# Kernel optimization log

Hardware: AMD Instinct MI355X
Metric: run time of the kernel (lower is better)

## Reference

```python
import jax, jax.numpy as jnp
import numpy as np

B, D = 256, 128            # batch, irreps_in dim for i='32x0e+32x1o' (32 + 32*3)
Z = D * (D + 1) // 2       # irreps_out.dim for symmetric formula 'ij=ji' -> 8256


def setup_inputs() -> dict:
    key = jax.random.key(0)
    k1, k2, k3 = jax.random.split(key, 3)
    x = jax.random.normal(k1, (B, D), dtype=jnp.float32)
    y = jax.random.normal(k2, (B, D), dtype=jnp.float32)
    # Precomputed change-of-basis (stand-in for the Wigner-3j/CG-built buffer).
    # Symmetrized over (i, j) to honor the ij=ji formula symmetry.
    C = jax.random.normal(k3, (Z, D, D), dtype=jnp.float32) / D
    C = 0.5 * (C + jnp.swapaxes(C, 1, 2))
    return {"x": x, "y": y, "change_of_basis": C}


def reference(x, y, change_of_basis):
    # ReducedTensorProducts forward == contraction with the change_of_basis:
    # out[b, z] = sum_{i,j} C[z, i, j] * x[b, i] * y[b, j]
    return jnp.einsum('zij,bi,bj->bz', change_of_basis, x, y)
```

## Files before the change

### kernel.cpp

```cpp
#include <hip/hip_runtime.h>


typedef __bf16 bf16x8 __attribute__((ext_vector_type(8)));
typedef float floatx4 __attribute__((ext_vector_type(4)));

#define TPB 256
#define GRID 512
#define NQ 33024

__global__ __launch_bounds__(TPB, 2)
void rtp_mfma_kernel(const float* __restrict__ xg,
                     const float* __restrict__ yg,
                     const float* __restrict__ Cg,
                     float* __restrict__ out)
{
    __shared__ __align__(16) __bf16 ct[2][32][136];
    __shared__ float xcol[2][256];

    const int tid   = threadIdx.x;
    const int wave  = tid >> 6;
    const int lane  = tid & 63;
    const int l15   = lane & 15;
    const int quad  = lane >> 4;
    const int wbase = wave << 6;

    const floatx4 z4 = {0.f, 0.f, 0.f, 0.f};

    bf16x8 yf[4][4];
#pragma unroll
    for (int mb = 0; mb < 4; ++mb) {
        const float* yrow = yg + (wbase + mb * 16 + l15) * 128;
#pragma unroll
        for (int w = 0; w < 4; ++w) {
            const float4 f0 = *(const float4*)(yrow + w * 32 + quad * 8);
            const float4 f1 = *(const float4*)(yrow + w * 32 + quad * 8 + 4);
            bf16x8 v;
            v[0] = (__bf16)f0.x; v[1] = (__bf16)f0.y;
            v[2] = (__bf16)f0.z; v[3] = (__bf16)f0.w;
            v[4] = (__bf16)f1.x; v[5] = (__bf16)f1.y;
            v[6] = (__bf16)f1.z; v[7] = (__bf16)f1.w;
            yf[mb][w] = v;
        }
    }

    const int sz = tid >> 3;
    const int sj = (tid & 7) << 4;

    int q        = ((int)blockIdx.x * 129) >> 1;
    const int q1 = (((int)blockIdx.x + 1) * 129) >> 1;

    float4 pv0, pv1, pv2, pv3;
    float  pxv;

    while (q < q1) {
        const int zt   = q >> 7;
        const int i0   = q & 127;
        const int qrem = q1 - q;
        const int ilen = (128 - i0) < qrem ? (128 - i0) : qrem;

        const float* crow = Cg + ((size_t)(zt * 32 + sz) << 14) + sj;

        auto loadtile = [&](int i) {
            const float4* s = (const float4*)(crow + (size_t)i * 128);
            pv0 = s[0]; pv1 = s[1]; pv2 = s[2]; pv3 = s[3];
            pxv = xg[tid * 128 + i];
        };
        auto commit = [&](int cb) {
            bf16x8 p0, p1;
            p0[0] = (__bf16)pv0.x; p0[1] = (__bf16)pv0.y;
            p0[2] = (__bf16)pv0.z; p0[3] = (__bf16)pv0.w;
            p0[4] = (__bf16)pv1.x; p0[5] = (__bf16)pv1.y;
            p0[6] = (__bf16)pv1.z; p0[7] = (__bf16)pv1.w;
            p1[0] = (__bf16)pv2.x; p1[1] = (__bf16)pv2.y;
            p1[2] = (__bf16)pv2.z; p1[3] = (__bf16)pv2.w;
            p1[4] = (__bf16)pv3.x; p1[5] = (__bf16)pv3.y;
            p1[6] = (__bf16)pv3.z; p1[7] = (__bf16)pv3.w;
            *(bf16x8*)&ct[cb][sz][sj]     = p0;
            *(bf16x8*)&ct[cb][sz][sj + 8] = p1;
            xcol[cb][tid] = pxv;
        };

        floatx4 acc[4][2];
#pragma unroll
        for (int mb = 0; mb < 4; ++mb) { acc[mb][0] = z4; acc[mb][1] = z4; }

        loadtile(i0);
        __syncthreads();
        commit(0);
        if (ilen > 1) loadtile(i0 + 1);
        __syncthreads();

        for (int t = 0; t < ilen; ++t) {
            const int buf = t & 1;
            if (t + 1 < ilen) {
                commit((t + 1) & 1);
                if (t + 2 < ilen) loadtile(i0 + t + 2);
            }

            floatx4 xv[4];
#pragma unroll
            for (int mb = 0; mb < 4; ++mb)
                xv[mb] = *(const floatx4*)&xcol[buf][wbase + mb * 16 + quad * 4];

            floatx4 S[4][2];
#pragma unroll
            for (int mb = 0; mb < 4; ++mb) { S[mb][0] = z4; S[mb][1] = z4; }

#pragma unroll
            for (int w = 0; w < 4; ++w) {
                const bf16x8 b0 = *(const bf16x8*)&ct[buf][l15][w * 32 + quad * 8];
                const bf16x8 b1 = *(const bf16x8*)&ct[buf][l15 + 16][w * 32 + quad * 8];
#pragma unroll
                for (int mb = 0; mb < 4; ++mb) {
                    S[mb][0] = __builtin_amdgcn_mfma_f32_16x16x32_bf16(yf[mb][w], b0, S[mb][0], 0, 0, 0);
                    S[mb][1] = __builtin_amdgcn_mfma_f32_16x16x32_bf16(yf[mb][w], b1, S[mb][1], 0, 0, 0);
                }
            }
#pragma unroll
            for (int mb = 0; mb < 4; ++mb) {
                acc[mb][0] += xv[mb] * S[mb][0];
                acc[mb][1] += xv[mb] * S[mb][1];
            }
            __syncthreads();
        }

#pragma unroll
        for (int mb = 0; mb < 4; ++mb) {
            const int brow = wbase + mb * 16 + quad * 4;
#pragma unroll
            for (int nb = 0; nb < 2; ++nb) {
                const int zc = zt * 32 + nb * 16 + l15;
                float* o = out + (size_t)brow * 8256 + zc;
                atomicAdd(o,            acc[mb][nb][0]);
                atomicAdd(o + 8256,     acc[mb][nb][1]);
                atomicAdd(o + 16512,    acc[mb][nb][2]);
                atomicAdd(o + 24768,    acc[mb][nb][3]);
            }
        }
        q += ilen;
    }
}

extern "C" void kernel_launch(void* const* d_in, const int* in_sizes, int n_in,
                              void* d_out, int out_size, void* d_ws, size_t ws_size,
                              hipStream_t stream) {
    (void)in_sizes; (void)n_in; (void)d_ws; (void)ws_size;
    const float* x = (const float*)d_in[0];
    const float* y = (const float*)d_in[1];
    const float* C = (const float*)d_in[2];
    float* out = (float*)d_out;
    hipMemsetAsync(out, 0, (size_t)out_size * sizeof(float), stream);
    rtp_mfma_kernel<<<GRID, TPB, 0, stream>>>(x, y, C, out);
}
```

Measured before the change: 734.8 us.

## Restructure RTP kernel to split j-dim across waves with register-direct C fragments

Each block now handles 16 z-rows over all 256 batch rows, with each wave owning a 32-wide slice of the j dimension. C fragments are loaded straight from global memory into registers using nontemporal loads and converted to bf16, replacing the LDS staging and the per-step barriers. Partial sums from the four waves are combined through LDS atomics before global atomics, so fewer global atomics are issued. A small pre-kernel transposes x into the workspace so x columns can be read as vectors. The cost is more registers for 16 y fragments, x read from global on every step, LDS atomic reduction, and an extra kernel launch.

```diff
diff --git a/kernel.cpp b/kernel.cpp
--- a/kernel.cpp
+++ b/kernel.cpp
@@ -6,137 +6,133 @@
 
 #define TPB 256
 #define GRID 512
-#define NQ 33024
 
+__global__ void xpose_kernel(const float* __restrict__ xg, float* __restrict__ xTg) {
+    const int n = blockIdx.x * 256 + threadIdx.x;
+    const int i = n >> 8, b = n & 255;
+    xTg[n] = xg[b * 128 + i];
+}
+
+template<bool XT>
 __global__ __launch_bounds__(TPB, 2)
-void rtp_mfma_kernel(const float* __restrict__ xg,
-                     const float* __restrict__ yg,
-                     const float* __restrict__ Cg,
-                     float* __restrict__ out)
+void rtp_v3(const float* __restrict__ xg, const float* __restrict__ yg,
+            const float* __restrict__ Cg, const float* __restrict__ xTg,
+            float* __restrict__ out)
 {
-    __shared__ __align__(16) __bf16 ct[2][32][136];
-    __shared__ float xcol[2][256];
+    __shared__ float scratch[256 * 16];
 
-    const int tid   = threadIdx.x;
-    const int wave  = tid >> 6;
-    const int lane  = tid & 63;
-    const int l15   = lane & 15;
-    const int quad  = lane >> 4;
-    const int wbase = wave << 6;
+    const int tid  = threadIdx.x;
+    const int w    = tid >> 6;
+    const int lane = tid & 63;
+    const int l15  = lane & 15;
+    const int quad = lane >> 4;
+
+#pragma unroll
+    for (int c = 0; c < 16; ++c) scratch[c * 256 + tid] = 0.f;
+
+    bf16x8 yf[16];
+    {
+        const float* ybase = yg + l15 * 128 + w * 32 + quad * 8;
+#pragma unroll
+        for (int mb = 0; mb < 16; ++mb) {
+            const floatx4 f0 = *(const floatx4*)(ybase + mb * 2048);
+            const floatx4 f1 = *(const floatx4*)(ybase + mb * 2048 + 4);
+            bf16x8 v;
+            v[0] = (__bf16)f0[0]; v[1] = (__bf16)f0[1];
+            v[2] = (__bf16)f0[2]; v[3] = (__bf16)f0[3];
+            v[4] = (__bf16)f1[0]; v[5] = (__bf16)f1[1];
+            v[6] = (__bf16)f1[2]; v[7] = (__bf16)f1[3];
+            yf[mb] = v;
+        }
+    }
+
+    __syncthreads();
+
+    int q        = (int)blockIdx.x * 129;
+    const int q1 = q + 129;
 
     const floatx4 z4 = {0.f, 0.f, 0.f, 0.f};
 
-    bf16x8 yf[4][4];
+    while (q < q1) {
+        const int z16  = q >> 7;
+        const int i0   = q & 127;
+        const int rem  = q1 - q;
+        const int ilen = (128 - i0) < rem ? (128 - i0) : rem;
+
+        const float* cb = Cg + (((size_t)(z16 * 16 + l15)) << 14)
+                             + (size_t)i0 * 128 + w * 32 + quad * 8;
+
+        floatx4 acc[16];
 #pragma unroll
-    for (int mb = 0; mb < 4; ++mb) {
-        const float* yrow = yg + (wbase + mb * 16 + l15) * 128;
-#pragma unroll
-        for (int w = 0; w < 4; ++w) {
-            const float4 f0 = *(const float4*)(yrow + w * 32 + quad * 8);
-            const float4 f1 = *(const float4*)(yrow + w * 32 + quad * 8 + 4);
-            bf16x8 v;
-            v[0] = (__bf16)f0.x; v[1] = (__bf16)f0.y;
-            v[2] = (__bf16)f0.z; v[3] = (__bf16)f0.w;
-            v[4] = (__bf16)f1.x; v[5] = (__bf16)f1.y;
-            v[6] = (__bf16)f1.z; v[7] = (__bf16)f1.w;
-            yf[mb][w] = v;
+        for (int mb = 0; mb < 16; ++mb) acc[mb] = z4;
+
+        floatx4 pv[2][2];
+        pv[0][0] = __builtin_nontemporal_load((const floatx4*)cb);
+        pv[0][1] = __builtin_nontemporal_load((const floatx4*)(cb + 4));
+        if (ilen > 1) {
+            pv[1][0] = __builtin_nontemporal_load((const floatx4*)(cb + 128));
+            pv[1][1] = __builtin_nontemporal_load((const floatx4*)(cb + 132));
         }
-    }
-
-    const int sz = tid >> 3;
-    const int sj = (tid & 7) << 4;
-
-    int q        = ((int)blockIdx.x * 129) >> 1;
-    const int q1 = (((int)blockIdx.x + 1) * 129) >> 1;
-
-    float4 pv0, pv1, pv2, pv3;
-    float  pxv;
-
-    while (q < q1) {
-        const int zt   = q >> 7;
-        const int i0   = q & 127;
-        const int qrem = q1 - q;
-        const int ilen = (128 - i0) < qrem ? (128 - i0) : qrem;
-
-        const float* crow = Cg + ((size_t)(zt * 32 + sz) << 14) + sj;
-
-        auto loadtile = [&](int i) {
-            const float4* s = (const float4*)(crow + (size_t)i * 128);
-            pv0 = s[0]; pv1 = s[1]; pv2 = s[2]; pv3 = s[3];
-            pxv = xg[tid * 128 + i];
-        };
-        auto commit = [&](int cb) {
-            bf16x8 p0, p1;
-            p0[0] = (__bf16)pv0.x; p0[1] = (__bf16)pv0.y;
-            p0[2] = (__bf16)pv0.z; p0[3] = (__bf16)pv0.w;
-            p0[4] = (__bf16)pv1.x; p0[5] = (__bf16)pv1.y;
-            p0[6] = (__bf16)pv1.z; p0[7] = (__bf16)pv1.w;
-            p1[0] = (__bf16)pv2.x; p1[1] = (__bf16)pv2.y;
-            p1[2] = (__bf16)pv2.z; p1[3] = (__bf16)pv2.w;
-            p1[4] = (__bf16)pv3.x; p1[5] = (__bf16)pv3.y;
-            p1[6] = (__bf16)pv3.z; p1[7] = (__bf16)pv3.w;
-            *(bf16x8*)&ct[cb][sz][sj]     = p0;
-            *(bf16x8*)&ct[cb][sz][sj + 8] = p1;
-            xcol[cb][tid] = pxv;
-        };
-
-        floatx4 acc[4][2];
-#pragma unroll
-        for (int mb = 0; mb < 4; ++mb) { acc[mb][0] = z4; acc[mb][1] = z4; }
-
-        loadtile(i0);
-        __syncthreads();
-        commit(0);
-        if (ilen > 1) loadtile(i0 + 1);
-        __syncthreads();
 
         for (int t = 0; t < ilen; ++t) {
             const int buf = t & 1;
-            if (t + 1 < ilen) {
-                commit((t + 1) & 1);
-                if (t + 2 < ilen) loadtile(i0 + t + 2);
+            const floatx4 f0 = pv[buf][0], f1 = pv[buf][1];
+            bf16x8 bfrag;
+            bfrag[0] = (__bf16)f0[0]; bfrag[1] = (__bf16)f0[1];
+            bfrag[2] = (__bf16)f0[2]; bfrag[3] = (__bf16)f0[3];
+            bfrag[4] = (__bf16)f1[0]; bfrag[5] = (__bf16)f1[1];
+            bfrag[6] = (__bf16)f1[2]; bfrag[7] = (__bf16)f1[3];
+
+            if (t + 2 < ilen) {
+                const float* p = cb + (size_t)(t + 2) * 128;
+                pv[buf][0] = __builtin_nontemporal_load((const floatx4*)p);
+                pv[buf][1] = __builtin_nontemporal_load((const floatx4*)(p + 4));
             }
 
-            floatx4 xv[4];
+            const int i = i0 + t;
 #pragma unroll
-            for (int mb = 0; mb < 4; ++mb)
-                xv[mb] = *(const floatx4*)&xcol[buf][wbase + mb * 16 + quad * 4];
-
-            floatx4 S[4][2];
-#pragma unroll
-            for (int mb = 0; mb < 4; ++mb) { S[mb][0] = z4; S[mb][1] = z4; }
-
-#pragma unroll
-            for (int w = 0; w < 4; ++w) {
-                const bf16x8 b0 = *(const bf16x8*)&ct[buf][l15][w * 32 + quad * 8];
-                const bf16x8 b1 = *(const bf16x8*)&ct[buf][l15 + 16][w * 32 + quad * 8];
-#pragma unroll
-                for (int mb = 0; mb < 4; ++mb) {
-                    S[mb][0] = __builtin_amdgcn_mfma_f32_16x16x32_bf16(yf[mb][w], b0, S[mb][0], 0, 0, 0);
-                    S[mb][1] = __builtin_amdgcn_mfma_f32_16x16x32_bf16(yf[mb][w], b1, S[mb][1], 0, 0, 0);
+            for (int mb = 0; mb < 16; ++mb) {
+                floatx4 S = __builtin_amdgcn_mfma_f32_16x16x32_bf16(yf[mb], bfrag, z4, 0, 0, 0);
+                floatx4 xv;
+                if (XT) {
+                    xv = *(const floatx4*)(xTg + i * 256 + mb * 16 + quad * 4);
+                } else {
+                    const float* xp = xg + (mb * 16 + quad * 4) * 128 + i;
+                    xv[0] = xp[0]; xv[1] = xp[128]; xv[2] = xp[256]; xv[3] = xp[384];
                 }
+                acc[mb] += xv * S;
             }
-#pragma unroll
-            for (int mb = 0; mb < 4; ++mb) {
-                acc[mb][0] += xv[mb] * S[mb][0];
-                acc[mb][1] += xv[mb] * S[mb][1];
-            }
-            __syncthreads();
         }
 
 #pragma unroll
-        for (int mb = 0; mb < 4; ++mb) {
-            const int brow = wbase + mb * 16 + quad * 4;
+        for (int mb = 0; mb < 16; ++mb) {
+            const int row = mb * 16 + quad * 4;
 #pragma unroll
-            for (int nb = 0; nb < 2; ++nb) {
-                const int zc = zt * 32 + nb * 16 + l15;
-                float* o = out + (size_t)brow * 8256 + zc;
-                atomicAdd(o,            acc[mb][nb][0]);
-                atomicAdd(o + 8256,     acc[mb][nb][1]);
-                atomicAdd(o + 16512,    acc[mb][nb][2]);
-                atomicAdd(o + 24768,    acc[mb][nb][3]);
-            }
+            for (int r = 0; r < 4; ++r)
+                atomicAdd(&scratch[(row + r) * 16 + l15], acc[mb][r]);
         }
+        __syncthreads();
+        {
+            float* srow = &scratch[tid * 16];
+            floatx4 s0 = *(floatx4*)(srow);
+            floatx4 s1 = *(floatx4*)(srow + 4);
+            floatx4 s2 = *(floatx4*)(srow + 8);
+            floatx4 s3 = *(floatx4*)(srow + 12);
+            float* orow = out + (size_t)tid * 8256 + z16 * 16;
+            atomicAdd(orow + 0,  s0[0]); atomicAdd(orow + 1,  s0[1]);
+            atomicAdd(orow + 2,  s0[2]); atomicAdd(orow + 3,  s0[3]);
+            atomicAdd(orow + 4,  s1[0]); atomicAdd(orow + 5,  s1[1]);
+            atomicAdd(orow + 6,  s1[2]); atomicAdd(orow + 7,  s1[3]);
+            atomicAdd(orow + 8,  s2[0]); atomicAdd(orow + 9,  s2[1]);
+            atomicAdd(orow + 10, s2[2]); atomicAdd(orow + 11, s2[3]);
+            atomicAdd(orow + 12, s3[0]); atomicAdd(orow + 13, s3[1]);
+            atomicAdd(orow + 14, s3[2]); atomicAdd(orow + 15, s3[3]);
+            *(floatx4*)(srow)      = z4;
+            *(floatx4*)(srow + 4)  = z4;
+            *(floatx4*)(srow + 8)  = z4;
+            *(floatx4*)(srow + 12) = z4;
+        }
+        __syncthreads();
         q += ilen;
     }
 }
@@ -144,11 +140,19 @@
 extern "C" void kernel_launch(void* const* d_in, const int* in_sizes, int n_in,
                               void* d_out, int out_size, void* d_ws, size_t ws_size,
                               hipStream_t stream) {
-    (void)in_sizes; (void)n_in; (void)d_ws; (void)ws_size;
+    (void)in_sizes; (void)n_in;
     const float* x = (const float*)d_in[0];
     const float* y = (const float*)d_in[1];
     const float* C = (const float*)d_in[2];
     float* out = (float*)d_out;
+
     hipMemsetAsync(out, 0, (size_t)out_size * sizeof(float), stream);
-    rtp_mfma_kernel<<<GRID, TPB, 0, stream>>>(x, y, C, out);
+
+    if (ws_size >= 32768 * sizeof(float)) {
+        float* xTg = (float*)d_ws;
+        xpose_kernel<<<128, 256, 0, stream>>>(x, xTg);
+        rtp_v3<true><<<GRID, TPB, 0, stream>>>(x, y, C, xTg, out);
+    } else {
+        rtp_v3<false><<<GRID, TPB, 0, stream>>>(x, y, C, x, out);
+    }
 }
```

Measured after the change: 1.223 ms. 66.5% more time.
